# Kernel optimization log

Measured on AMD Instinct MI355X. Metric: run time of the kernel, lower is better.

Reference implementation:

```python
import jax, jax.numpy as jnp
import numpy as np

TAU = 20.0
THRESHOLD = 1.0
RESET_V = 0.0
DT = 1.0
SIM_TIME = 100


def setup_inputs() -> dict:
    key = jax.random.key(0)
    ks = jax.random.split(key, 6)
    B, D, H, A = 8192, 256, 256, 64
    return {
        "x": jax.random.normal(ks[0], (B, D), dtype=jnp.float32),
        "enc_W": jax.random.normal(ks[1], (D, D), dtype=jnp.float32) * 0.1,  # Linear weight [out,in]
        "enc_b": jnp.zeros((D,), dtype=jnp.float32),
        "W1": jax.random.normal(ks[2], (D, H), dtype=jnp.float32) * 0.1,
        "W2": jax.random.normal(ks[3], (H, H), dtype=jnp.float32) * 0.1,
        "W3": jax.random.normal(ks[4], (H, A), dtype=jnp.float32) * 0.1,
    }


def _lif_step(v, inp, W, decay):
    # synaptic input -> leaky integrate -> fire -> reset
    syn = inp @ W
    v = v * decay + syn * (1.0 - decay)
    spikes = (v >= THRESHOLD).astype(v.dtype)
    v = jnp.where(spikes > 0, RESET_V, v)
    return v, spikes


def reference(x, enc_W, enc_b, W1, W2, W3):
    B = x.shape[0]
    decay = jnp.exp(jnp.asarray(-DT / TAU, dtype=x.dtype))
    # rate encoding: sigmoid(Linear(x)); constant input at every timestep
    rates = jax.nn.sigmoid(x @ enc_W.T + enc_b)

    H1, H2, A = W1.shape[1], W2.shape[1], W3.shape[1]
    init = (
        jnp.zeros((B, H1), x.dtype),
        jnp.zeros((B, H2), x.dtype),
        jnp.zeros((B, A), x.dtype),
        jnp.zeros((B, A), x.dtype),  # accumulated output spikes
    )

    def step(carry, _):
        v1, v2, v3, acc = carry
        v1, s1 = _lif_step(v1, rates, W1, decay)
        v2, s2 = _lif_step(v2, s1, W2, decay)
        v3, s3 = _lif_step(v3, s2, W3, decay)
        return (v1, v2, v3, acc + s3), None

    (_, _, _, acc), _ = jax.lax.scan(step, init, None, length=SIM_TIME)
    return acc / SIM_TIME
```

## Files before the change

### kernel.cpp

```cpp
#include <hip/hip_runtime.h>
#include <math.h>

#define SIM_T 100

__global__ __launch_bounds__(256) void k_prep(const float* __restrict__ encW,
                                              float* __restrict__ encWT,
                                              const float4* __restrict__ x4,
                                              float4* __restrict__ xp4) {
  int bid = blockIdx.x;
  int t = threadIdx.x;
  if (bid < 256) {
    encWT[bid * 256 + t] = encW[t * 256 + bid];
  } else {
    int id = (bid - 256) * 256 + t;
    int k4 = id >> 13, b = id & 8191;
    xp4[id] = x4[(size_t)b * 64 + k4];
  }
}

template <int EPI>
__global__ __launch_bounds__(256, 2) void k_gemm_ws(
    const float4* __restrict__ Ap,
    const float* __restrict__ WT,
    const float* __restrict__ bias,
    float4* __restrict__ Op,
    float omd) {
  const int lane = threadIdx.x & 63;
  const int wvS = __builtin_amdgcn_readfirstlane(threadIdx.x >> 6);
  const int btile = blockIdx.x & 127;
  const int cb = blockIdx.x >> 7;
  const int b = btile * 64 + lane;
  const int colbase = cb * 64 + wvS * 16;
  const float* wp = WT + colbase;
  const float4* Ab = Ap + b;

  float acc[16];
#pragma unroll
  for (int c = 0; c < 16; c++) acc[c] = 0.f;

#pragma unroll 4
  for (int k4 = 0; k4 < 64; k4++) {
    float4 a = Ab[(size_t)k4 * 8192];
    const float* af = &a.x;
#pragma unroll
    for (int kk = 0; kk < 4; kk++) {
      const float* wk = wp + (k4 * 4 + kk) * 256;
#pragma unroll
      for (int c = 0; c < 16; c++) acc[c] = fmaf(af[kk], wk[c], acc[c]);
    }
  }

#pragma unroll
  for (int j = 0; j < 4; j++) {
    float4 o;
    float* of = &o.x;
    if (EPI == 0) {
#pragma unroll
      for (int q = 0; q < 4; q++) {
        float v = acc[j * 4 + q] + bias[colbase + j * 4 + q];
        of[q] = 1.f / (1.f + expf(-v));
      }
    } else {
#pragma unroll
      for (int q = 0; q < 4; q++) of[q] = __fmul_rn(acc[j * 4 + q], omd);
    }
    Op[(size_t)((colbase >> 2) + j) * 8192 + b] = o;
  }
}

__global__ __launch_bounds__(256, 8) void k_sim(
    const float4* __restrict__ cp4,
    const float* __restrict__ W2,
    const float* __restrict__ W3,
    float* __restrict__ out, float decay, float omd) {
  const int lane = threadIdx.x & 63;
  const int row = blockIdx.x * 4 + (threadIdx.x >> 6);
  float4 cv = cp4[(size_t)lane * 8192 + row];
  const float c0 = cv.x, c1 = cv.y, c2 = cv.z, c3 = cv.w;
  float v10 = 0.f, v11 = 0.f, v12 = 0.f, v13 = 0.f;
  float v20 = 0.f, v21 = 0.f, v22 = 0.f, v23 = 0.f;
  float v3 = 0.f;
  int acc = 0;
  const float4* w2q = (const float4*)W2 + lane;
  const float* w3q = W3 + lane;

  for (int t = 0; t < SIM_T; t++) {
    v10 = fmaf(v10, decay, c0);
    bool f0 = v10 >= 1.f;
    unsigned long long m0 = __ballot(f0);
    v10 = f0 ? 0.f : v10;
    v11 = fmaf(v11, decay, c1);
    bool f1 = v11 >= 1.f;
    unsigned long long m1 = __ballot(f1);
    v11 = f1 ? 0.f : v11;
    v12 = fmaf(v12, decay, c2);
    bool f2 = v12 >= 1.f;
    unsigned long long m2 = __ballot(f2);
    v12 = f2 ? 0.f : v12;
    v13 = fmaf(v13, decay, c3);
    bool f3 = v13 >= 1.f;
    unsigned long long m3 = __ballot(f3);
    v13 = f3 ? 0.f : v13;

    float s0 = 0.f, s1 = 0.f, s2 = 0.f, s3 = 0.f;
#define ACC2(mask, q)                             \
  {                                               \
    unsigned long long m = (mask);                \
    while (m) {                                   \
      int i = __builtin_ctzll(m);                 \
      m &= m - 1;                                 \
      float4 w = w2q[i * 256 + (q) * 64];         \
      s0 += w.x;                                  \
      s1 += w.y;                                  \
      s2 += w.z;                                  \
      s3 += w.w;                                  \
    }                                             \
  }
    ACC2(m0, 0)
    ACC2(m1, 1)
    ACC2(m2, 2)
    ACC2(m3, 3)

    v20 = fmaf(v20, decay, __fmul_rn(s0, omd));
    bool g0 = v20 >= 1.f;
    unsigned long long n0 = __ballot(g0);
    v20 = g0 ? 0.f : v20;
    v21 = fmaf(v21, decay, __fmul_rn(s1, omd));
    bool g1 = v21 >= 1.f;
    unsigned long long n1 = __ballot(g1);
    v21 = g1 ? 0.f : v21;
    v22 = fmaf(v22, decay, __fmul_rn(s2, omd));
    bool g2 = v22 >= 1.f;
    unsigned long long n2 = __ballot(g2);
    v22 = g2 ? 0.f : v22;
    v23 = fmaf(v23, decay, __fmul_rn(s3, omd));
    bool g3 = v23 >= 1.f;
    unsigned long long n3 = __ballot(g3);
    v23 = g3 ? 0.f : v23;

    float z = 0.f;
    if (n0 | n1 | n2 | n3) {
#define ACC3(mask, q)                             \
  {                                               \
    unsigned long long m = (mask);                \
    while (m) {                                   \
      int i = __builtin_ctzll(m);                 \
      m &= m - 1;                                 \
      z += w3q[(i * 4 + (q)) * 64];               \
    }                                             \
  }
      ACC3(n0, 0)
      ACC3(n1, 1)
      ACC3(n2, 2)
      ACC3(n3, 3)
    }
    v3 = fmaf(v3, decay, __fmul_rn(z, omd));
    bool h = v3 >= 1.f;
    acc += h ? 1 : 0;
    v3 = h ? 0.f : v3;
  }
  out[(size_t)row * 64 + lane] = __fdiv_rn((float)acc, 100.f);
}

extern "C" void kernel_launch(void* const* d_in, const int* in_sizes, int n_in,
                              void* d_out, int out_size, void* d_ws,
                              size_t ws_size, hipStream_t stream) {
  const float* x = (const float*)d_in[0];
  const float* encW = (const float*)d_in[1];
  const float* encB = (const float*)d_in[2];
  const float* W1 = (const float*)d_in[3];
  const float* W2 = (const float*)d_in[4];
  const float* W3 = (const float*)d_in[5];
  float* out = (float*)d_out;

  float4* xp4 = (float4*)d_ws;
  float4* rates_p4 = (float4*)((float*)d_ws + 2097152);
  float* encWT = (float*)d_ws + 4194304;

  const float decay = (float)exp((double)(-0.05f));
  const float omd = 1.0f - decay;

  k_prep<<<2304, 256, 0, stream>>>(encW, encWT, (const float4*)x, xp4);
  k_gemm_ws<0><<<512, 256, 0, stream>>>(xp4, encWT, encB, rates_p4, omd);
  k_gemm_ws<1><<<512, 256, 0, stream>>>(rates_p4, W1, encB, xp4, omd);
  k_sim<<<2048, 256, 0, stream>>>((const float4*)xp4, W2, W3, out, decay, omd);
}
```

Baseline: 181.1 us.

## Fuse encoder and first-layer GEMMs into the simulation kernel

The two separate GEMM kernels (encoder with sigmoid, then W1 with scaling) and the x re-layout pass are folded into the simulation kernel. Each wavefront now computes its own row's rates and layer-1 drive, with the rates exchanged through shared memory. This drops two launches and the global round trips for the rates and drive tensors. In exchange, each wave does a row-per-wave dot product that reloads the weights for every row, giving less register reuse than the tiled GEMM.

```diff
diff --git a/kernel.cpp b/kernel.cpp
--- a/kernel.cpp
+++ b/kernel.cpp
@@ -3,80 +3,94 @@
 
 #define SIM_T 100
 
-__global__ __launch_bounds__(256) void k_prep(const float* __restrict__ encW,
-                                              float* __restrict__ encWT,
-                                              const float4* __restrict__ x4,
-                                              float4* __restrict__ xp4) {
-  int bid = blockIdx.x;
-  int t = threadIdx.x;
-  if (bid < 256) {
-    encWT[bid * 256 + t] = encW[t * 256 + bid];
-  } else {
-    int id = (bid - 256) * 256 + t;
-    int k4 = id >> 13, b = id & 8191;
-    xp4[id] = x4[(size_t)b * 64 + k4];
-  }
+__global__ __launch_bounds__(256) void k_transpose256(
+    const float* __restrict__ W, float* __restrict__ WT) {
+  int k = blockIdx.x;
+  int o = threadIdx.x;
+  WT[k * 256 + o] = W[o * 256 + k];
 }
 
-template <int EPI>
-__global__ __launch_bounds__(256, 2) void k_gemm_ws(
-    const float4* __restrict__ Ap,
-    const float* __restrict__ WT,
-    const float* __restrict__ bias,
-    float4* __restrict__ Op,
-    float omd) {
-  const int lane = threadIdx.x & 63;
-  const int wvS = __builtin_amdgcn_readfirstlane(threadIdx.x >> 6);
-  const int btile = blockIdx.x & 127;
-  const int cb = blockIdx.x >> 7;
-  const int b = btile * 64 + lane;
-  const int colbase = cb * 64 + wvS * 16;
-  const float* wp = WT + colbase;
-  const float4* Ab = Ap + b;
-
-  float acc[16];
-#pragma unroll
-  for (int c = 0; c < 16; c++) acc[c] = 0.f;
-
-#pragma unroll 4
-  for (int k4 = 0; k4 < 64; k4++) {
-    float4 a = Ab[(size_t)k4 * 8192];
-    const float* af = &a.x;
-#pragma unroll
-    for (int kk = 0; kk < 4; kk++) {
-      const float* wk = wp + (k4 * 4 + kk) * 256;
-#pragma unroll
-      for (int c = 0; c < 16; c++) acc[c] = fmaf(af[kk], wk[c], acc[c]);
-    }
-  }
-
-#pragma unroll
-  for (int j = 0; j < 4; j++) {
-    float4 o;
-    float* of = &o.x;
-    if (EPI == 0) {
-#pragma unroll
-      for (int q = 0; q < 4; q++) {
-        float v = acc[j * 4 + q] + bias[colbase + j * 4 + q];
-        of[q] = 1.f / (1.f + expf(-v));
-      }
-    } else {
-#pragma unroll
-      for (int q = 0; q < 4; q++) of[q] = __fmul_rn(acc[j * 4 + q], omd);
-    }
-    Op[(size_t)((colbase >> 2) + j) * 8192 + b] = o;
-  }
-}
-
-__global__ __launch_bounds__(256, 8) void k_sim(
-    const float4* __restrict__ cp4,
+__global__ __launch_bounds__(256, 8) void k_mega(
+    const float* __restrict__ x,
+    const float* __restrict__ encWT,
+    const float* __restrict__ encB,
+    const float* __restrict__ W1,
     const float* __restrict__ W2,
     const float* __restrict__ W3,
     float* __restrict__ out, float decay, float omd) {
+  __shared__ float4 shr[4 * 64];
   const int lane = threadIdx.x & 63;
-  const int row = blockIdx.x * 4 + (threadIdx.x >> 6);
-  float4 cv = cp4[(size_t)lane * 8192 + row];
-  const float c0 = cv.x, c1 = cv.y, c2 = cv.z, c3 = cv.w;
+  const int w = threadIdx.x >> 6;
+  const int row = blockIdx.x * 4 + w;
+
+  const float4* Wt4 = (const float4*)encWT + lane;
+  const float* xr = x + (size_t)row * 256;
+  float a0 = 0.f, a1 = 0.f, a2 = 0.f, a3 = 0.f;
+#pragma unroll 4
+  for (int k4 = 0; k4 < 64; k4++) {
+    float4 xv = *(const float4*)(xr + k4 * 4);
+    float4 w0 = Wt4[(k4 * 4 + 0) * 64];
+    float4 w1 = Wt4[(k4 * 4 + 1) * 64];
+    float4 w2 = Wt4[(k4 * 4 + 2) * 64];
+    float4 w3 = Wt4[(k4 * 4 + 3) * 64];
+    a0 = fmaf(xv.x, w0.x, a0);
+    a1 = fmaf(xv.x, w0.y, a1);
+    a2 = fmaf(xv.x, w0.z, a2);
+    a3 = fmaf(xv.x, w0.w, a3);
+    a0 = fmaf(xv.y, w1.x, a0);
+    a1 = fmaf(xv.y, w1.y, a1);
+    a2 = fmaf(xv.y, w1.z, a2);
+    a3 = fmaf(xv.y, w1.w, a3);
+    a0 = fmaf(xv.z, w2.x, a0);
+    a1 = fmaf(xv.z, w2.y, a1);
+    a2 = fmaf(xv.z, w2.z, a2);
+    a3 = fmaf(xv.z, w2.w, a3);
+    a0 = fmaf(xv.w, w3.x, a0);
+    a1 = fmaf(xv.w, w3.y, a1);
+    a2 = fmaf(xv.w, w3.z, a2);
+    a3 = fmaf(xv.w, w3.w, a3);
+  }
+  {
+    float4 bv = ((const float4*)encB)[lane];
+    float4 rq;
+    rq.x = 1.f / (1.f + expf(-(a0 + bv.x)));
+    rq.y = 1.f / (1.f + expf(-(a1 + bv.y)));
+    rq.z = 1.f / (1.f + expf(-(a2 + bv.z)));
+    rq.w = 1.f / (1.f + expf(-(a3 + bv.w)));
+    shr[w * 64 + lane] = rq;
+  }
+
+  const float4* W14 = (const float4*)W1 + lane;
+  a0 = a1 = a2 = a3 = 0.f;
+#pragma unroll 4
+  for (int k4 = 0; k4 < 64; k4++) {
+    float4 rv = shr[w * 64 + k4];
+    float4 w0 = W14[(k4 * 4 + 0) * 64];
+    float4 w1 = W14[(k4 * 4 + 1) * 64];
+    float4 w2 = W14[(k4 * 4 + 2) * 64];
+    float4 w3 = W14[(k4 * 4 + 3) * 64];
+    a0 = fmaf(rv.x, w0.x, a0);
+    a1 = fmaf(rv.x, w0.y, a1);
+    a2 = fmaf(rv.x, w0.z, a2);
+    a3 = fmaf(rv.x, w0.w, a3);
+    a0 = fmaf(rv.y, w1.x, a0);
+    a1 = fmaf(rv.y, w1.y, a1);
+    a2 = fmaf(rv.y, w1.z, a2);
+    a3 = fmaf(rv.y, w1.w, a3);
+    a0 = fmaf(rv.z, w2.x, a0);
+    a1 = fmaf(rv.z, w2.y, a1);
+    a2 = fmaf(rv.z, w2.z, a2);
+    a3 = fmaf(rv.z, w2.w, a3);
+    a0 = fmaf(rv.w, w3.x, a0);
+    a1 = fmaf(rv.w, w3.y, a1);
+    a2 = fmaf(rv.w, w3.z, a2);
+    a3 = fmaf(rv.w, w3.w, a3);
+  }
+  const float c0 = __fmul_rn(a0, omd);
+  const float c1 = __fmul_rn(a1, omd);
+  const float c2 = __fmul_rn(a2, omd);
+  const float c3 = __fmul_rn(a3, omd);
+
   float v10 = 0.f, v11 = 0.f, v12 = 0.f, v13 = 0.f;
   float v20 = 0.f, v21 = 0.f, v22 = 0.f, v23 = 0.f;
   float v3 = 0.f;
@@ -109,11 +123,11 @@
     while (m) {                                   \
       int i = __builtin_ctzll(m);                 \
       m &= m - 1;                                 \
-      float4 w = w2q[i * 256 + (q) * 64];         \
-      s0 += w.x;                                  \
-      s1 += w.y;                                  \
-      s2 += w.z;                                  \
-      s3 += w.w;                                  \
+      float4 wv = w2q[i * 256 + (q) * 64];        \
+      s0 += wv.x;                                 \
+      s1 += wv.y;                                 \
+      s2 += wv.z;                                 \
+      s3 += wv.w;                                 \
     }                                             \
   }
     ACC2(m0, 0)
@@ -173,15 +187,12 @@
   const float* W3 = (const float*)d_in[5];
   float* out = (float*)d_out;
 
-  float4* xp4 = (float4*)d_ws;
-  float4* rates_p4 = (float4*)((float*)d_ws + 2097152);
-  float* encWT = (float*)d_ws + 4194304;
+  float* encWT = (float*)d_ws;
 
   const float decay = (float)exp((double)(-0.05f));
   const float omd = 1.0f - decay;
 
-  k_prep<<<2304, 256, 0, stream>>>(encW, encWT, (const float4*)x, xp4);
-  k_gemm_ws<0><<<512, 256, 0, stream>>>(xp4, encWT, encB, rates_p4, omd);
-  k_gemm_ws<1><<<512, 256, 0, stream>>>(rates_p4, W1, encB, xp4, omd);
-  k_sim<<<2048, 256, 0, stream>>>((const float4*)xp4, W2, W3, out, decay, omd);
+  k_transpose256<<<256, 256, 0, stream>>>(encW, encWT);
+  k_mega<<<2048, 256, 0, stream>>>(x, encWT, encB, W1, W2, W3, out, decay,
+                                   omd);
 }
```

Result: slower. 246.9 us (+36.3%).
